# Kernel optimization log

Hardware: AMD Instinct MI355X
Metric: run time of the kernel (lower is better)

## Reference

```python
import jax, jax.numpy as jnp
import numpy as np

N_NODES = 100000
IN_CH = 128
HID = 64
N_EDGES = 1600000
NEG_SLOPE = 0.2


def setup_inputs() -> dict:
    key = jax.random.key(0)
    k1, k2, k3, k4, k5, k6 = jax.random.split(key, 6)
    x = jax.random.normal(k1, (N_NODES, IN_CH), dtype=jnp.float32)
    edge_index = jax.random.randint(k2, (2, N_EDGES), 0, N_NODES, dtype=jnp.int64)
    # Glorot-style init for GATConv params (heads=1)
    s_w = (2.0 / (IN_CH + HID)) ** 0.5
    W = jax.random.normal(k3, (IN_CH, HID), dtype=jnp.float32) * s_w
    s_a = (2.0 / (1 + HID)) ** 0.5
    att_src = jax.random.normal(k4, (HID,), dtype=jnp.float32) * s_a
    att_dst = jax.random.normal(k5, (HID,), dtype=jnp.float32) * s_a
    bias = jnp.zeros((HID,), dtype=jnp.float32)
    return {"x": x, "edge_index": edge_index, "W": W, "att_src": att_src,
            "att_dst": att_dst, "bias": bias}


def reference(x, edge_index, W, att_src, att_dst, bias):
    N = x.shape[0]
    # PyG GATConv default: add self-loops
    loop = jnp.arange(N, dtype=edge_index.dtype)
    src = jnp.concatenate([edge_index[0], loop])  # message source j
    dst = jnp.concatenate([edge_index[1], loop])  # message target i

    h = x @ W                      # [N, HID]
    a_src = h @ att_src            # [N]
    a_dst = h @ att_dst            # [N]

    # per-edge attention logit: LeakyReLU(a_src[j] + a_dst[i])
    e = jax.nn.leaky_relu(a_src[src] + a_dst[dst], NEG_SLOPE)  # [E+N]
    # numerically-stable segment softmax over destination node
    m = jax.ops.segment_max(e, dst, num_segments=N)
    e = jnp.exp(e - m[dst])
    denom = jax.ops.segment_sum(e, dst, num_segments=N)
    alpha = e / (denom[dst] + 1e-16)               # [E+N]

    # scatter-aggregate weighted source features, then bias
    out = jax.ops.segment_sum(alpha[:, None] * h[src], dst, num_segments=N)
    out = out + bias               # [N, HID]
    return out, alpha[:, None]     # alpha shaped [E+N, heads=1]
```

## Files before the change

### kernel.cpp

```cpp
#include <hip/hip_runtime.h>

#define NN 100000
#define IC 128
#define HD 64
#define NEG 0.2f
#define NPB 32
#define NBKT (NN / NPB)
#define CAP 768
#define TILE 4096
#define NIT 8

__device__ __forceinline__ float bf16u_to_f32(unsigned short u) {
  union { unsigned int i; float f; } v;
  v.i = ((unsigned int)u) << 16;
  return v.f;
}

__device__ __forceinline__ unsigned short f32_to_bf16u(float f) {
  union { float f; unsigned int i; } v;
  v.f = f;
  unsigned int b = v.i;
  b += 0x7FFFu + ((b >> 16) & 1u);
  return (unsigned short)(b >> 16);
}

__global__ __launch_bounds__(256) void k_gemm(const float* __restrict__ x,
                                              const float* __restrict__ W,
                                              const float* __restrict__ att_s,
                                              const float* __restrict__ att_d,
                                              unsigned short* __restrict__ hb,
                                              float* __restrict__ as_,
                                              float* __restrict__ ad_,
                                              int* __restrict__ bktcur) {
  __shared__ float xs[IC][64];
  __shared__ float wsm[IC][HD];
  const int tid = threadIdx.x;
  const int n0 = blockIdx.x * 64;
  if (tid < 2 && 2 * blockIdx.x + tid < NBKT) bktcur[2 * blockIdx.x + tid] = 0;

  #pragma unroll
  for (int i = 0; i < 8; ++i) {
    int f = i * 256 + tid;
    int k = f >> 4, c = (f & 15) << 2;
    *(float4*)&wsm[k][c] = *(const float4*)&W[k * HD + c];
  }
  #pragma unroll
  for (int i = 0; i < 8; ++i) {
    int f = i * 256 + tid;
    int r = f >> 5, k0 = (f & 31) << 2;
    float4 v = make_float4(0.f, 0.f, 0.f, 0.f);
    if (n0 + r < NN) v = *(const float4*)&x[(size_t)(n0 + r) * IC + k0];
    const float* vf = (const float*)&v;
    #pragma unroll
    for (int j = 0; j < 4; ++j) {
      int k = k0 + j;
      int sw = ((k >> 2) & 7) << 2;
      xs[k][r ^ sw] = vf[j];
    }
  }
  __syncthreads();

  const int c0 = (tid & 15) << 2;
  const int r0 = (tid >> 4) << 2;
  float acc[4][4] = {};
  #pragma unroll 4
  for (int k = 0; k < IC; ++k) {
    int sw = ((k >> 2) & 7) << 2;
    float4 xv = *(float4*)&xs[k][r0 ^ sw];
    float4 wv = *(float4*)&wsm[k][c0];
    float xa[4] = {xv.x, xv.y, xv.z, xv.w};
    float wa[4] = {wv.x, wv.y, wv.z, wv.w};
    #pragma unroll
    for (int a = 0; a < 4; ++a)
      #pragma unroll
      for (int b = 0; b < 4; ++b) acc[a][b] += xa[a] * wa[b];
  }

  float as4[4], ad4[4];
  #pragma unroll
  for (int j = 0; j < 4; ++j) { as4[j] = att_s[c0 + j]; ad4[j] = att_d[c0 + j]; }

  #pragma unroll
  for (int a = 0; a < 4; ++a) {
    int n = n0 + r0 + a;
    float ps = acc[a][0]*as4[0] + acc[a][1]*as4[1] + acc[a][2]*as4[2] + acc[a][3]*as4[3];
    float pd = acc[a][0]*ad4[0] + acc[a][1]*ad4[1] + acc[a][2]*ad4[2] + acc[a][3]*ad4[3];
    #pragma unroll
    for (int mk = 1; mk < 16; mk <<= 1) {
      ps += __shfl_xor(ps, mk);
      pd += __shfl_xor(pd, mk);
    }
    if (n < NN) {
      ushort4 hv;
      hv.x = f32_to_bf16u(acc[a][0]);
      hv.y = f32_to_bf16u(acc[a][1]);
      hv.z = f32_to_bf16u(acc[a][2]);
      hv.w = f32_to_bf16u(acc[a][3]);
      *(ushort4*)&hb[(size_t)n * HD + c0] = hv;
      if ((tid & 15) == 0) { as_[n] = ps; ad_[n] = pd; }
    }
  }
}

__global__ __launch_bounds__(512) void k_part(const int* __restrict__ ei,
                                              const float* __restrict__ as_,
                                              const float* __restrict__ ad_,
                                              int* __restrict__ bktcur,
                                              int2* __restrict__ bktbuf,
                                              float* __restrict__ p_lin,
                                              int E, int M) {
  __shared__ int lcnt[NBKT];
  __shared__ int gbs[NBKT];
  const int tid = threadIdx.x;
  const int base = blockIdx.x * TILE;

  for (int c = tid; c < NBKT; c += 512) lcnt[c] = 0;
  __syncthreads();

  int pkx[NIT], rb[NIT];
  float tv[NIT];
  #pragma unroll
  for (int i = 0; i < NIT; ++i) {
    int m = base + i * 512 + tid;
    if (m < M) {
      int s, d;
      if (m < E) { s = ei[m]; d = ei[E + m]; }
      else       { s = m - E; d = s; }
      int b = d >> 5;
      pkx[i] = (s << 5) | (d & 31);
      tv[i] = as_[s] + ad_[d];
      int r = atomicAdd(&lcnt[b], 1);
      rb[i] = (b << 12) | r;
    } else rb[i] = -1;
  }
  __syncthreads();

  for (int c = tid; c < NBKT; c += 512) {
    int v = lcnt[c];
    gbs[c] = v ? atomicAdd(&bktcur[c], v) : 0;
  }
  __syncthreads();

  #pragma unroll
  for (int i = 0; i < NIT; ++i) {
    if (rb[i] >= 0) {
      int m = base + i * 512 + tid;
      float t = tv[i];
      t = t > 0.f ? t : NEG * t;
      float p = __expf(t);
      p_lin[m] = p;
      int b = (unsigned)rb[i] >> 12, r = rb[i] & 4095;
      int slot = gbs[b] + r;
      if (slot < CAP)
        bktbuf[(size_t)b * CAP + slot] = make_int2(pkx[i], __float_as_int(p));
    }
  }
}

__global__ __launch_bounds__(256) void k_pg(const int* __restrict__ bktcur,
                                            const int2* __restrict__ bktbuf,
                                            const unsigned short* __restrict__ hb,
                                            const float* __restrict__ bias,
                                            float* __restrict__ out,
                                            float* __restrict__ denom) {
  __shared__ int2 sp[CAP];
  __shared__ int cnt2[NPB], nstart[NPB], cur[NPB];
  __shared__ float dls[NPB];
  const int b = blockIdx.x;
  const int d0 = b << 5;
  const int tid = threadIdx.x;
  const int cnt = min(bktcur[b], CAP);
  const int2* mybuf = bktbuf + (size_t)b * CAP;
  const char* hbb = (const char*)hb;

  if (tid < NPB) cnt2[tid] = 0;
  __syncthreads();
  for (int e = tid; e < cnt; e += 256) atomicAdd(&cnt2[mybuf[e].x & 31], 1);
  __syncthreads();

  if (tid < 32) {
    int a = cnt2[tid];
    int va = a;
    #pragma unroll
    for (int off = 1; off < 32; off <<= 1) {
      int na = __shfl_up(va, off);
      if (tid >= off) va += na;
    }
    nstart[tid] = va - a;
    cur[tid] = va - a;
  }
  __syncthreads();
  for (int e = tid; e < cnt; e += 256) {
    int2 v = mybuf[e];
    int slot = atomicAdd(&cur[v.x & 31], 1);
    sp[slot] = make_int2((v.x & ~31) << 2, v.y);
  }
  __syncthreads();

  const int wv = tid >> 6, lane = tid & 63;
  const unsigned chb = (unsigned)lane << 1;
  const float bs = bias[lane];
  for (int n = wv; n < NPB; n += 4) {
    int beg = nstart[n], end = beg + cnt2[n];
    float acc = 0.f, dens = 0.f;
    int e = beg;
    for (; e + 3 < end; e += 4) {
      int2 v0 = sp[e], v1 = sp[e + 1], v2 = sp[e + 2], v3 = sp[e + 3];
      unsigned short h0 = *(const unsigned short*)(hbb + ((unsigned)v0.x + chb));
      unsigned short h1 = *(const unsigned short*)(hbb + ((unsigned)v1.x + chb));
      unsigned short h2 = *(const unsigned short*)(hbb + ((unsigned)v2.x + chb));
      unsigned short h3 = *(const unsigned short*)(hbb + ((unsigned)v3.x + chb));
      float p0 = __int_as_float(v0.y), p1 = __int_as_float(v1.y);
      float p2 = __int_as_float(v2.y), p3 = __int_as_float(v3.y);
      dens += (p0 + p1) + (p2 + p3);
      acc += p0 * bf16u_to_f32(h0) + p1 * bf16u_to_f32(h1);
      acc += p2 * bf16u_to_f32(h2) + p3 * bf16u_to_f32(h3);
    }
    for (; e < end; ++e) {
      int2 v0 = sp[e];
      float p0 = __int_as_float(v0.y);
      dens += p0;
      acc += p0 * bf16u_to_f32(*(const unsigned short*)(hbb + ((unsigned)v0.x + chb)));
    }
    out[(size_t)(d0 + n) * HD + lane] = acc / (dens + 1e-16f) + bs;
    if (lane == 0) dls[n] = dens;
  }
  __syncthreads();
  if (tid < NPB) denom[d0 + tid] = dls[tid];
}

__global__ __launch_bounds__(256) void k_alpha(const int* __restrict__ ei,
                                               const float* __restrict__ p_lin,
                                               const float* __restrict__ denom,
                                               float* __restrict__ alpha_out,
                                               int E, int M) {
  int m = blockIdx.x * 256 + threadIdx.x;
  if (m >= M) return;
  int d = (m < E) ? ei[E + m] : (m - E);
  alpha_out[m] = p_lin[m] / (denom[d] + 1e-16f);
}

extern "C" void kernel_launch(void* const* d_in, const int* in_sizes, int n_in,
                              void* d_out, int out_size, void* d_ws, size_t ws_size,
                              hipStream_t stream) {
  const float* x     = (const float*)d_in[0];
  const int*   ei    = (const int*)d_in[1];
  const float* W     = (const float*)d_in[2];
  const float* att_s = (const float*)d_in[3];
  const float* att_d = (const float*)d_in[4];
  const float* bias  = (const float*)d_in[5];

  const int E = in_sizes[1] / 2;
  const int M = E + NN;

  float* out       = (float*)d_out;
  float* alpha_out = out + (size_t)NN * HD;

  char* w = (char*)d_ws;
  auto alloc = [&](size_t bytes) {
    char* p = w;
    w += (bytes + 15) & ~(size_t)15;
    return p;
  };
  unsigned short* hb = (unsigned short*)alloc(sizeof(unsigned short) * (size_t)NN * HD);
  float* as_    = (float*)alloc(sizeof(float) * NN);
  float* ad_    = (float*)alloc(sizeof(float) * NN);
  float* denom  = (float*)alloc(sizeof(float) * NN);
  float* p_lin  = (float*)alloc(sizeof(float) * (size_t)M);
  int*   bktcur = (int*)alloc(sizeof(int) * NBKT);
  int2*  bktbuf = (int2*)alloc(sizeof(int2) * (size_t)NBKT * CAP);

  k_gemm<<<(NN + 63) / 64, 256, 0, stream>>>(x, W, att_s, att_d, hb, as_, ad_,
                                             bktcur);
  k_part<<<(M + TILE - 1) / TILE, 512, 0, stream>>>(ei, as_, ad_, bktcur,
                                                    bktbuf, p_lin, E, M);
  k_pg<<<NBKT, 256, 0, stream>>>(bktcur, bktbuf, hb, bias, out, denom);
  k_alpha<<<(M + 255) / 256, 256, 0, stream>>>(ei, p_lin, denom, alpha_out,
                                               E, M);
}
```

Baseline: 132.1 us.

## Compute node projection GEMM with bf16 MFMA instead of FP32 FMAs

Replaces the scalar FP32 outer-product GEMM in the projection kernel with bf16 MFMA 16x16x32 instructions. x and W are converted to bf16 in swizzled shared memory, with W stored transposed. Outputs are staged through shared memory so each node's row is written to global with coalesced stores. This cuts ALU time in the GEMM stage, but the inputs are now rounded to bf16, which lowers the precision of h and of the attention logits.

```diff
diff --git a/kernel.cpp b/kernel.cpp
--- a/kernel.cpp
+++ b/kernel.cpp
@@ -10,6 +10,9 @@
 #define TILE 4096
 #define NIT 8
 
+typedef float f32x4 __attribute__((ext_vector_type(4)));
+typedef short s16x8 __attribute__((ext_vector_type(8)));
+
 __device__ __forceinline__ float bf16u_to_f32(unsigned short u) {
   union { unsigned int i; float f; } v;
   v.i = ((unsigned int)u) << 16;
@@ -32,72 +35,98 @@
                                               float* __restrict__ as_,
                                               float* __restrict__ ad_,
                                               int* __restrict__ bktcur) {
-  __shared__ float xs[IC][64];
-  __shared__ float wsm[IC][HD];
+  __shared__ unsigned short xb[64 * 128];
+  __shared__ unsigned short wt[64 * 128];
   const int tid = threadIdx.x;
   const int n0 = blockIdx.x * 64;
   if (tid < 2 && 2 * blockIdx.x + tid < NBKT) bktcur[2 * blockIdx.x + tid] = 0;
 
-  #pragma unroll
-  for (int i = 0; i < 8; ++i) {
-    int f = i * 256 + tid;
-    int k = f >> 4, c = (f & 15) << 2;
-    *(float4*)&wsm[k][c] = *(const float4*)&W[k * HD + c];
-  }
   #pragma unroll
   for (int i = 0; i < 8; ++i) {
     int f = i * 256 + tid;
     int r = f >> 5, k0 = (f & 31) << 2;
     float4 v = make_float4(0.f, 0.f, 0.f, 0.f);
     if (n0 + r < NN) v = *(const float4*)&x[(size_t)(n0 + r) * IC + k0];
+    ushort4 u;
+    u.x = f32_to_bf16u(v.x); u.y = f32_to_bf16u(v.y);
+    u.z = f32_to_bf16u(v.z); u.w = f32_to_bf16u(v.w);
+    int idx = r * 128 + k0;
+    *(ushort4*)&xb[idx ^ ((r & 7) << 3)] = u;
+  }
+  #pragma unroll
+  for (int i = 0; i < 8; ++i) {
+    int f = i * 256 + tid;
+    int k = f >> 4, c0 = (f & 15) << 2;
+    float4 v = *(const float4*)&W[k * HD + c0];
     const float* vf = (const float*)&v;
     #pragma unroll
     for (int j = 0; j < 4; ++j) {
-      int k = k0 + j;
-      int sw = ((k >> 2) & 7) << 2;
-      xs[k][r ^ sw] = vf[j];
-    }
-  }
-  __syncthreads();
-
-  const int c0 = (tid & 15) << 2;
-  const int r0 = (tid >> 4) << 2;
-  float acc[4][4] = {};
-  #pragma unroll 4
-  for (int k = 0; k < IC; ++k) {
-    int sw = ((k >> 2) & 7) << 2;
-    float4 xv = *(float4*)&xs[k][r0 ^ sw];
-    float4 wv = *(float4*)&wsm[k][c0];
-    float xa[4] = {xv.x, xv.y, xv.z, xv.w};
-    float wa[4] = {wv.x, wv.y, wv.z, wv.w};
-    #pragma unroll
-    for (int a = 0; a < 4; ++a)
-      #pragma unroll
-      for (int b = 0; b < 4; ++b) acc[a][b] += xa[a] * wa[b];
-  }
-
-  float as4[4], ad4[4];
-  #pragma unroll
-  for (int j = 0; j < 4; ++j) { as4[j] = att_s[c0 + j]; ad4[j] = att_d[c0 + j]; }
-
-  #pragma unroll
-  for (int a = 0; a < 4; ++a) {
-    int n = n0 + r0 + a;
-    float ps = acc[a][0]*as4[0] + acc[a][1]*as4[1] + acc[a][2]*as4[2] + acc[a][3]*as4[3];
-    float pd = acc[a][0]*ad4[0] + acc[a][1]*ad4[1] + acc[a][2]*ad4[2] + acc[a][3]*ad4[3];
+      int c = c0 + j;
+      int idx = c * 128 + k;
+      wt[idx ^ ((c & 7) << 3)] = f32_to_bf16u(vf[j]);
+    }
+  }
+  __syncthreads();
+
+  const int wv = tid >> 6, lane = tid & 63;
+  const int fr = lane & 15;
+  const int fq = lane >> 4;
+  const int nodeR = wv * 16 + fr;
+  f32x4 acc[4] = {};
+  #pragma unroll
+  for (int kb = 0; kb < 4; ++kb) {
+    int ks = kb * 32 + fq * 8;
+    int ia = nodeR * 128 + ks;
+    s16x8 af = *(s16x8*)&xb[ia ^ ((nodeR & 7) << 3)];
+    #pragma unroll
+    for (int cg = 0; cg < 4; ++cg) {
+      int col = cg * 16 + fr;
+      int ib = col * 128 + ks;
+      s16x8 bfr = *(s16x8*)&wt[ib ^ ((col & 7) << 3)];
+      acc[cg] = __builtin_amdgcn_mfma_f32_16x16x32_bf16(af, bfr, acc[cg], 0, 0, 0);
+    }
+  }
+
+  float atts[4], attd[4];
+  #pragma unroll
+  for (int cg = 0; cg < 4; ++cg) {
+    atts[cg] = att_s[cg * 16 + fr];
+    attd[cg] = att_d[cg * 16 + fr];
+  }
+  __syncthreads();
+  unsigned short* ho = xb;
+
+  #pragma unroll
+  for (int j = 0; j < 4; ++j) {
+    int nrel = wv * 16 + fq * 4 + j;
+    float ps = acc[0][j]*atts[0] + acc[1][j]*atts[1]
+             + acc[2][j]*atts[2] + acc[3][j]*atts[3];
+    float pd = acc[0][j]*attd[0] + acc[1][j]*attd[1]
+             + acc[2][j]*attd[2] + acc[3][j]*attd[3];
     #pragma unroll
     for (int mk = 1; mk < 16; mk <<= 1) {
       ps += __shfl_xor(ps, mk);
       pd += __shfl_xor(pd, mk);
     }
-    if (n < NN) {
-      ushort4 hv;
-      hv.x = f32_to_bf16u(acc[a][0]);
-      hv.y = f32_to_bf16u(acc[a][1]);
-      hv.z = f32_to_bf16u(acc[a][2]);
-      hv.w = f32_to_bf16u(acc[a][3]);
-      *(ushort4*)&hb[(size_t)n * HD + c0] = hv;
-      if ((tid & 15) == 0) { as_[n] = ps; ad_[n] = pd; }
+    if (fr == 0 && n0 + nrel < NN) { as_[n0 + nrel] = ps; ad_[n0 + nrel] = pd; }
+    #pragma unroll
+    for (int cg = 0; cg < 4; ++cg)
+      ho[nrel * 72 + cg * 16 + fr] = f32_to_bf16u(acc[cg][j]);
+  }
+  __syncthreads();
+
+  {
+    int node = tid >> 2, ch = (tid & 3) << 4;
+    if (n0 + node < NN) {
+      ushort4 a0 = *(ushort4*)&ho[node * 72 + ch];
+      ushort4 a1 = *(ushort4*)&ho[node * 72 + ch + 4];
+      ushort4 a2 = *(ushort4*)&ho[node * 72 + ch + 8];
+      ushort4 a3 = *(ushort4*)&ho[node * 72 + ch + 12];
+      unsigned short* dst = &hb[(size_t)(n0 + node) * HD + ch];
+      *(ushort4*)(dst) = a0;
+      *(ushort4*)(dst + 4) = a1;
+      *(ushort4*)(dst + 8) = a2;
+      *(ushort4*)(dst + 12) = a3;
     }
   }
 }
```

Result: faster. 116.1 us (-12.1%).
